# Performance work log

Measured on AMD Instinct MI355X. Metric: run time of the kernel, lower is better.

Reference implementation:

```python
import jax, jax.numpy as jnp
import numpy as np

DIM_CODES = 512
DICT_SIZE = 512
EMBED_DIM = 16
BATCH = 512


def setup_inputs() -> dict:
    key = jax.random.key(0)
    k1, k2 = jax.random.split(key)
    mu = jax.random.normal(k1, (BATCH, DIM_CODES * EMBED_DIM), dtype=jnp.float32)
    dictionary = jax.random.normal(k2, (DIM_CODES, DICT_SIZE, EMBED_DIM), dtype=jnp.float32)
    return {"mu": mu, "dictionary": dictionary}


def reference(mu, dictionary):
    # mu: [B, C*E], dictionary: [C, K, E]
    B = mu.shape[0]
    C, K, E = dictionary.shape
    mu3 = mu.reshape(B, C, E)
    # pairwise squared distance ||mu - d||^2 = ||mu||^2 + ||d||^2 - 2 mu.d -> [B, C, K]
    dist = (jnp.sum(mu3 * mu3, axis=-1)[..., None]
            + jnp.sum(dictionary * dictionary, axis=-1)[None]
            - 2.0 * jnp.einsum('bce,cke->bck', mu3, dictionary))
    idx = jnp.argmin(dist, axis=-1)  # [B, C] int
    # gather nearest codebook entries: per-code index into its own codebook
    z_embed = dictionary[jnp.arange(C)[None, :], idx]  # [B, C, E]
    z_embed = z_embed.reshape(B, C * E)
    # TransferGrad: forward = z_embed, backward passes grad straight-through to mu
    z = mu + jax.lax.stop_gradient(z_embed - mu)
    one_hot_idx = jax.nn.one_hot(idx, K, dtype=mu.dtype)  # [B, C, K]
    return z, z_embed, one_hot_idx
```

## Files before the change

kernel.cpp:

```cpp
#include <hip/hip_runtime.h>
#include <float.h>

constexpr int C    = 512;
constexpr int K    = 512;
constexpr int E    = 16;
constexpr int B    = 512;
constexpr int RB   = 256;
constexpr int MUS  = C * E;

typedef float f32x4 __attribute__((ext_vector_type(4)));

__launch_bounds__(256, 4)
__global__ void vq_scan(const float* __restrict__ mu,
                        const float* __restrict__ dict,
                        float* __restrict__ z,
                        float* __restrict__ zq,
                        int*   __restrict__ idx_t)
{
    const int c    = blockIdx.x;
    const int b0   = blockIdx.y * RB;
    const int tid  = threadIdx.x;
    const int lane = tid & 63;
    const int wave = tid >> 6;

    __shared__ __align__(16) float dict_s[K * E];
    __shared__ float nrm_s[K];

    const float* __restrict__ dbase = dict + (size_t)c * K * E;

#pragma unroll
    for (int rep = 0; rep < 2; ++rep) {
        const int k = tid + rep * 256;
        const float4* p = reinterpret_cast<const float4*>(dbase + k * E);
        const float4 d0 = p[0], d1 = p[1], d2 = p[2], d3 = p[3];
        float s = d0.x * d0.x;
        s = fmaf(d0.y, d0.y, s); s = fmaf(d0.z, d0.z, s); s = fmaf(d0.w, d0.w, s);
        s = fmaf(d1.x, d1.x, s); s = fmaf(d1.y, d1.y, s);
        s = fmaf(d1.z, d1.z, s); s = fmaf(d1.w, d1.w, s);
        s = fmaf(d2.x, d2.x, s); s = fmaf(d2.y, d2.y, s);
        s = fmaf(d2.z, d2.z, s); s = fmaf(d2.w, d2.w, s);
        s = fmaf(d3.x, d3.x, s); s = fmaf(d3.y, d3.y, s);
        s = fmaf(d3.z, d3.z, s); s = fmaf(d3.w, d3.w, s);
        float4* q4 = reinterpret_cast<float4*>(&dict_s[k * E]);
        q4[0] = d0; q4[1] = d1; q4[2] = d2; q4[3] = d3;
        nrm_s[k] = s;
    }
    __syncthreads();

    const int myrow = (wave << 6) + lane;
    const int b     = b0 + myrow;
    const float* __restrict__ mrow = mu + (size_t)b * MUS + c * E;
    float4 m0, m1, m2, m3;
    {
        const float4* p = reinterpret_cast<const float4*>(mrow);
        m0 = p[0]; m1 = p[1]; m2 = p[2]; m3 = p[3];
    }
    float nm = m0.x * m0.x;
    nm = fmaf(m0.y, m0.y, nm); nm = fmaf(m0.z, m0.z, nm); nm = fmaf(m0.w, m0.w, nm);
    nm = fmaf(m1.x, m1.x, nm); nm = fmaf(m1.y, m1.y, nm);
    nm = fmaf(m1.z, m1.z, nm); nm = fmaf(m1.w, m1.w, nm);
    nm = fmaf(m2.x, m2.x, nm); nm = fmaf(m2.y, m2.y, nm);
    nm = fmaf(m2.z, m2.z, nm); nm = fmaf(m2.w, m2.w, nm);
    nm = fmaf(m3.x, m3.x, nm); nm = fmaf(m3.y, m3.y, nm);
    nm = fmaf(m3.z, m3.z, nm); nm = fmaf(m3.w, m3.w, nm);

    float bd = FLT_MAX, sec = FLT_MAX;
    int   bk = K;
    const float4* __restrict__ ds4 = reinterpret_cast<const float4*>(dict_s);
#pragma unroll 4
    for (int k = 0; k < K; ++k) {
        const float4 d0 = ds4[k * 4 + 0];
        const float4 d1 = ds4[k * 4 + 1];
        const float4 d2 = ds4[k * 4 + 2];
        const float4 d3 = ds4[k * 4 + 3];
        float acc = d0.x * m0.x;
        acc = fmaf(d0.y, m0.y, acc); acc = fmaf(d0.z, m0.z, acc); acc = fmaf(d0.w, m0.w, acc);
        acc = fmaf(d1.x, m1.x, acc); acc = fmaf(d1.y, m1.y, acc);
        acc = fmaf(d1.z, m1.z, acc); acc = fmaf(d1.w, m1.w, acc);
        acc = fmaf(d2.x, m2.x, acc); acc = fmaf(d2.y, m2.y, acc);
        acc = fmaf(d2.z, m2.z, acc); acc = fmaf(d2.w, m2.w, acc);
        acc = fmaf(d3.x, m3.x, acc); acc = fmaf(d3.y, m3.y, acc);
        acc = fmaf(d3.z, m3.z, acc); acc = fmaf(d3.w, m3.w, acc);
        const float dist = fmaf(-2.0f, acc, nm + nrm_s[k]);
        const bool  lt   = dist < bd;
        sec = lt ? bd : fminf(sec, dist);
        bd  = lt ? dist : bd;
        bk  = lt ? k : bk;
    }

    unsigned long long trig = __ballot(sec < bd + 1e-3f);
    while (trig) {
        const int r = __ffsll(trig) - 1;
        trig &= trig - 1;
        const int row = (wave << 6) + r;
        const float* __restrict__ qrow = mu + (size_t)(b0 + row) * MUS + c * E;

        double nmuD = 0.0;
#pragma unroll
        for (int t = 0; t < E; ++t) {
            const double mt = (double)qrow[t];
            nmuD += mt * mt;
        }
        double bD = DBL_MAX;
        int    bK = K;
#pragma unroll
        for (int i = 0; i < 8; ++i) {
            const int k = lane + 64 * i;
            const float* dk = &dict_s[k * E];
            double nd = 0.0, dt = 0.0;
#pragma unroll
            for (int t = 0; t < 4; ++t) {
                const double dx = dk[4 * t + 0], dy = dk[4 * t + 1];
                const double dz = dk[4 * t + 2], dw = dk[4 * t + 3];
                const double mx = qrow[4 * t + 0], my = qrow[4 * t + 1];
                const double mz = qrow[4 * t + 2], mw = qrow[4 * t + 3];
                nd += dx * dx + dy * dy + dz * dz + dw * dw;
                dt += dx * mx + dy * my + dz * mz + dw * mw;
            }
            const double dist = nmuD + nd - 2.0 * dt;
            if (dist < bD) { bD = dist; bK = k; }
        }
#pragma unroll
        for (int off = 32; off; off >>= 1) {
            const double od = __shfl_down(bD, off);
            const int    ok = __shfl_down(bK, off);
            if (od < bD || (od == bD && ok < bK)) { bD = od; bK = ok; }
        }
        const int kwin = __shfl(bK, 0);
        if (lane == r) bk = kwin;
    }

    idx_t[c * B + b] = bk;

    {
        const float4* dwin = reinterpret_cast<const float4*>(&dict_s[bk * E]);
        const float4 q0 = dwin[0], q1 = dwin[1], q2 = dwin[2], q3 = dwin[3];
        float* zqp = zq + (size_t)b * MUS + (size_t)c * E;
        float* zp  = z  + (size_t)b * MUS + (size_t)c * E;
        reinterpret_cast<float4*>(zqp)[0] = q0;
        reinterpret_cast<float4*>(zqp)[1] = q1;
        reinterpret_cast<float4*>(zqp)[2] = q2;
        reinterpret_cast<float4*>(zqp)[3] = q3;
        float4 z0, z1, z2, z3;
        z0.x = m0.x + (q0.x - m0.x); z0.y = m0.y + (q0.y - m0.y);
        z0.z = m0.z + (q0.z - m0.z); z0.w = m0.w + (q0.w - m0.w);
        z1.x = m1.x + (q1.x - m1.x); z1.y = m1.y + (q1.y - m1.y);
        z1.z = m1.z + (q1.z - m1.z); z1.w = m1.w + (q1.w - m1.w);
        z2.x = m2.x + (q2.x - m2.x); z2.y = m2.y + (q2.y - m2.y);
        z2.z = m2.z + (q2.z - m2.z); z2.w = m2.w + (q2.w - m2.w);
        z3.x = m3.x + (q3.x - m3.x); z3.y = m3.y + (q3.y - m3.y);
        z3.z = m3.z + (q3.z - m3.z); z3.w = m3.w + (q3.w - m3.w);
        reinterpret_cast<float4*>(zp)[0] = z0;
        reinterpret_cast<float4*>(zp)[1] = z1;
        reinterpret_cast<float4*>(zp)[2] = z2;
        reinterpret_cast<float4*>(zp)[3] = z3;
    }
}

__launch_bounds__(256)
__global__ void vq_onehot(const int* __restrict__ idx_t,
                          float* __restrict__ oh)
{
    const long TOT = (long)B * C * K / 4;
    const long stride = (long)gridDim.x * blockDim.x;
    long f4 = (long)blockIdx.x * blockDim.x + threadIdx.x;
#pragma unroll 4
    for (; f4 < TOT; f4 += stride) {
        const int rowu = __builtin_amdgcn_readfirstlane((int)(f4 >> 7));
        const int bb   = rowu >> 9;
        const int cc   = rowu & (C - 1);
        const int kk   = idx_t[cc * B + bb];
        const int k0   = ((int)f4 & 127) << 2;
        f32x4 v;
        v.x = (k0 + 0 == kk) ? 1.0f : 0.0f;
        v.y = (k0 + 1 == kk) ? 1.0f : 0.0f;
        v.z = (k0 + 2 == kk) ? 1.0f : 0.0f;
        v.w = (k0 + 3 == kk) ? 1.0f : 0.0f;
        __builtin_nontemporal_store(v, reinterpret_cast<f32x4*>(oh) + f4);
    }
}

extern "C" void kernel_launch(void* const* d_in, const int* in_sizes, int n_in,
                              void* d_out, int out_size, void* d_ws, size_t ws_size,
                              hipStream_t stream)
{
    const float* mu   = (const float*)d_in[0];
    const float* dict = (const float*)d_in[1];

    float* z  = (float*)d_out;
    float* zq = z  + (size_t)B * C * E;
    float* oh = zq + (size_t)B * C * E;

    int* idx_t = (int*)d_ws;

    dim3 g1(C, B / RB);
    vq_scan<<<g1, 256, 0, stream>>>(mu, dict, z, zq, idx_t);
    vq_onehot<<<2048, 256, 0, stream>>>(idx_t, oh);
}
```

Before: 701.6 us.

## Register-block four batch rows per thread to reuse each LDS dictionary read

Each thread now handles four batch rows for one code, so every dictionary entry read from LDS feeds four dot products instead of one. The grid drops to one 128-thread block per code, and each block loads its codebook once rather than twice. This cuts LDS traffic per FMA and duplicated dictionary loads. In exchange it raises register pressure, reduces the total thread count to 64K, and lowers occupancy (launch bounds 128,1), which may hurt latency hiding.

```diff
diff --git a/kernel.cpp b/kernel.cpp
--- a/kernel.cpp
+++ b/kernel.cpp
@@ -5,12 +5,12 @@
 constexpr int K    = 512;
 constexpr int E    = 16;
 constexpr int B    = 512;
-constexpr int RB   = 256;
 constexpr int MUS  = C * E;
+constexpr int R    = 4;
 
 typedef float f32x4 __attribute__((ext_vector_type(4)));
 
-__launch_bounds__(256, 4)
+__launch_bounds__(128, 1)
 __global__ void vq_scan(const float* __restrict__ mu,
                         const float* __restrict__ dict,
                         float* __restrict__ z,
@@ -18,7 +18,6 @@
                         int*   __restrict__ idx_t)
 {
     const int c    = blockIdx.x;
-    const int b0   = blockIdx.y * RB;
     const int tid  = threadIdx.x;
     const int lane = tid & 63;
     const int wave = tid >> 6;
@@ -29,8 +28,8 @@
     const float* __restrict__ dbase = dict + (size_t)c * K * E;
 
 #pragma unroll
-    for (int rep = 0; rep < 2; ++rep) {
-        const int k = tid + rep * 256;
+    for (int rep = 0; rep < 4; ++rep) {
+        const int k = tid + rep * 128;
         const float4* p = reinterpret_cast<const float4*>(dbase + k * E);
         const float4 d0 = p[0], d1 = p[1], d2 = p[2], d3 = p[3];
         float s = d0.x * d0.x;
@@ -47,25 +46,33 @@
     }
     __syncthreads();
 
-    const int myrow = (wave << 6) + lane;
-    const int b     = b0 + myrow;
-    const float* __restrict__ mrow = mu + (size_t)b * MUS + c * E;
-    float4 m0, m1, m2, m3;
-    {
-        const float4* p = reinterpret_cast<const float4*>(mrow);
-        m0 = p[0]; m1 = p[1]; m2 = p[2]; m3 = p[3];
-    }
-    float nm = m0.x * m0.x;
-    nm = fmaf(m0.y, m0.y, nm); nm = fmaf(m0.z, m0.z, nm); nm = fmaf(m0.w, m0.w, nm);
-    nm = fmaf(m1.x, m1.x, nm); nm = fmaf(m1.y, m1.y, nm);
-    nm = fmaf(m1.z, m1.z, nm); nm = fmaf(m1.w, m1.w, nm);
-    nm = fmaf(m2.x, m2.x, nm); nm = fmaf(m2.y, m2.y, nm);
-    nm = fmaf(m2.z, m2.z, nm); nm = fmaf(m2.w, m2.w, nm);
-    nm = fmaf(m3.x, m3.x, nm); nm = fmaf(m3.y, m3.y, nm);
-    nm = fmaf(m3.z, m3.z, nm); nm = fmaf(m3.w, m3.w, nm);
-
-    float bd = FLT_MAX, sec = FLT_MAX;
-    int   bk = K;
+    float4 m[R][4];
+    float  nm[R];
+#pragma unroll
+    for (int s = 0; s < R; ++s) {
+        const int b = tid + 128 * s;
+        const float4* p = reinterpret_cast<const float4*>(
+            mu + (size_t)b * MUS + c * E);
+        m[s][0] = p[0]; m[s][1] = p[1]; m[s][2] = p[2]; m[s][3] = p[3];
+        float v = m[s][0].x * m[s][0].x;
+        v = fmaf(m[s][0].y, m[s][0].y, v);
+        v = fmaf(m[s][0].z, m[s][0].z, v);
+        v = fmaf(m[s][0].w, m[s][0].w, v);
+#pragma unroll
+        for (int t = 1; t < 4; ++t) {
+            v = fmaf(m[s][t].x, m[s][t].x, v);
+            v = fmaf(m[s][t].y, m[s][t].y, v);
+            v = fmaf(m[s][t].z, m[s][t].z, v);
+            v = fmaf(m[s][t].w, m[s][t].w, v);
+        }
+        nm[s] = v;
+    }
+
+    float bd[R], sec[R];
+    int   bk[R];
+#pragma unroll
+    for (int s = 0; s < R; ++s) { bd[s] = FLT_MAX; sec[s] = FLT_MAX; bk[s] = K; }
+
     const float4* __restrict__ ds4 = reinterpret_cast<const float4*>(dict_s);
 #pragma unroll 4
     for (int k = 0; k < K; ++k) {
@@ -73,67 +80,84 @@
         const float4 d1 = ds4[k * 4 + 1];
         const float4 d2 = ds4[k * 4 + 2];
         const float4 d3 = ds4[k * 4 + 3];
-        float acc = d0.x * m0.x;
-        acc = fmaf(d0.y, m0.y, acc); acc = fmaf(d0.z, m0.z, acc); acc = fmaf(d0.w, m0.w, acc);
-        acc = fmaf(d1.x, m1.x, acc); acc = fmaf(d1.y, m1.y, acc);
-        acc = fmaf(d1.z, m1.z, acc); acc = fmaf(d1.w, m1.w, acc);
-        acc = fmaf(d2.x, m2.x, acc); acc = fmaf(d2.y, m2.y, acc);
-        acc = fmaf(d2.z, m2.z, acc); acc = fmaf(d2.w, m2.w, acc);
-        acc = fmaf(d3.x, m3.x, acc); acc = fmaf(d3.y, m3.y, acc);
-        acc = fmaf(d3.z, m3.z, acc); acc = fmaf(d3.w, m3.w, acc);
-        const float dist = fmaf(-2.0f, acc, nm + nrm_s[k]);
-        const bool  lt   = dist < bd;
-        sec = lt ? bd : fminf(sec, dist);
-        bd  = lt ? dist : bd;
-        bk  = lt ? k : bk;
-    }
-
-    unsigned long long trig = __ballot(sec < bd + 1e-3f);
-    while (trig) {
-        const int r = __ffsll(trig) - 1;
-        trig &= trig - 1;
-        const int row = (wave << 6) + r;
-        const float* __restrict__ qrow = mu + (size_t)(b0 + row) * MUS + c * E;
-
-        double nmuD = 0.0;
-#pragma unroll
-        for (int t = 0; t < E; ++t) {
-            const double mt = (double)qrow[t];
-            nmuD += mt * mt;
+        const float  nr = nrm_s[k];
+#pragma unroll
+        for (int s = 0; s < R; ++s) {
+            float acc = d0.x * m[s][0].x;
+            acc = fmaf(d0.y, m[s][0].y, acc);
+            acc = fmaf(d0.z, m[s][0].z, acc);
+            acc = fmaf(d0.w, m[s][0].w, acc);
+            acc = fmaf(d1.x, m[s][1].x, acc);
+            acc = fmaf(d1.y, m[s][1].y, acc);
+            acc = fmaf(d1.z, m[s][1].z, acc);
+            acc = fmaf(d1.w, m[s][1].w, acc);
+            acc = fmaf(d2.x, m[s][2].x, acc);
+            acc = fmaf(d2.y, m[s][2].y, acc);
+            acc = fmaf(d2.z, m[s][2].z, acc);
+            acc = fmaf(d2.w, m[s][2].w, acc);
+            acc = fmaf(d3.x, m[s][3].x, acc);
+            acc = fmaf(d3.y, m[s][3].y, acc);
+            acc = fmaf(d3.z, m[s][3].z, acc);
+            acc = fmaf(d3.w, m[s][3].w, acc);
+            const float dist = fmaf(-2.0f, acc, nm[s] + nr);
+            const bool  lt   = dist < bd[s];
+            sec[s] = lt ? bd[s] : fminf(sec[s], dist);
+            bd[s]  = lt ? dist : bd[s];
+            bk[s]  = lt ? k : bk[s];
         }
-        double bD = DBL_MAX;
-        int    bK = K;
-#pragma unroll
-        for (int i = 0; i < 8; ++i) {
-            const int k = lane + 64 * i;
-            const float* dk = &dict_s[k * E];
-            double nd = 0.0, dt = 0.0;
-#pragma unroll
-            for (int t = 0; t < 4; ++t) {
-                const double dx = dk[4 * t + 0], dy = dk[4 * t + 1];
-                const double dz = dk[4 * t + 2], dw = dk[4 * t + 3];
-                const double mx = qrow[4 * t + 0], my = qrow[4 * t + 1];
-                const double mz = qrow[4 * t + 2], mw = qrow[4 * t + 3];
-                nd += dx * dx + dy * dy + dz * dz + dw * dw;
-                dt += dx * mx + dy * my + dz * mz + dw * mw;
+    }
+
+#pragma unroll
+    for (int s = 0; s < R; ++s) {
+        unsigned long long trig = __ballot(sec[s] < bd[s] + 1e-3f);
+        while (trig) {
+            const int r = __ffsll(trig) - 1;
+            trig &= trig - 1;
+            const int row = (wave << 6) + r + 128 * s;
+            const float* __restrict__ qrow = mu + (size_t)row * MUS + c * E;
+
+            double nmuD = 0.0;
+#pragma unroll
+            for (int t = 0; t < E; ++t) {
+                const double mt = (double)qrow[t];
+                nmuD += mt * mt;
             }
-            const double dist = nmuD + nd - 2.0 * dt;
-            if (dist < bD) { bD = dist; bK = k; }
+            double bD = DBL_MAX;
+            int    bK = K;
+#pragma unroll
+            for (int i = 0; i < 8; ++i) {
+                const int kk = lane + 64 * i;
+                const float* dk = &dict_s[kk * E];
+                double nd = 0.0, dt = 0.0;
+#pragma unroll
+                for (int t = 0; t < 4; ++t) {
+                    const double dx = dk[4 * t + 0], dy = dk[4 * t + 1];
+                    const double dz = dk[4 * t + 2], dw = dk[4 * t + 3];
+                    const double mx = qrow[4 * t + 0], my = qrow[4 * t + 1];
+                    const double mz = qrow[4 * t + 2], mw = qrow[4 * t + 3];
+                    nd += dx * dx + dy * dy + dz * dz + dw * dw;
+                    dt += dx * mx + dy * my + dz * mz + dw * mw;
+                }
+                const double dist = nmuD + nd - 2.0 * dt;
+                if (dist < bD) { bD = dist; bK = kk; }
+            }
+#pragma unroll
+            for (int off = 32; off; off >>= 1) {
+                const double od = __shfl_down(bD, off);
+                const int    ok = __shfl_down(bK, off);
+                if (od < bD || (od == bD && ok < bK)) { bD = od; bK = ok; }
+            }
+            const int kwin = __shfl(bK, 0);
+            if (lane == r) bk[s] = kwin;
         }
-#pragma unroll
-        for (int off = 32; off; off >>= 1) {
-            const double od = __shfl_down(bD, off);
-            const int    ok = __shfl_down(bK, off);
-            if (od < bD || (od == bD && ok < bK)) { bD = od; bK = ok; }
-        }
-        const int kwin = __shfl(bK, 0);
-        if (lane == r) bk = kwin;
-    }
-
-    idx_t[c * B + b] = bk;
-
-    {
-        const float4* dwin = reinterpret_cast<const float4*>(&dict_s[bk * E]);
+    }
+
+#pragma unroll
+    for (int s = 0; s < R; ++s) {
+        const int b = tid + 128 * s;
+        idx_t[c * B + b] = bk[s];
+
+        const float4* dwin = reinterpret_cast<const float4*>(&dict_s[bk[s] * E]);
         const float4 q0 = dwin[0], q1 = dwin[1], q2 = dwin[2], q3 = dwin[3];
         float* zqp = zq + (size_t)b * MUS + (size_t)c * E;
         float* zp  = z  + (size_t)b * MUS + (size_t)c * E;
@@ -142,14 +166,14 @@
         reinterpret_cast<float4*>(zqp)[2] = q2;
         reinterpret_cast<float4*>(zqp)[3] = q3;
         float4 z0, z1, z2, z3;
-        z0.x = m0.x + (q0.x - m0.x); z0.y = m0.y + (q0.y - m0.y);
-        z0.z = m0.z + (q0.z - m0.z); z0.w = m0.w + (q0.w - m0.w);
-        z1.x = m1.x + (q1.x - m1.x); z1.y = m1.y + (q1.y - m1.y);
-        z1.z = m1.z + (q1.z - m1.z); z1.w = m1.w + (q1.w - m1.w);
-        z2.x = m2.x + (q2.x - m2.x); z2.y = m2.y + (q2.y - m2.y);
-        z2.z = m2.z + (q2.z - m2.z); z2.w = m2.w + (q2.w - m2.w);
-        z3.x = m3.x + (q3.x - m3.x); z3.y = m3.y + (q3.y - m3.y);
-        z3.z = m3.z + (q3.z - m3.z); z3.w = m3.w + (q3.w - m3.w);
+        z0.x = m[s][0].x + (q0.x - m[s][0].x); z0.y = m[s][0].y + (q0.y - m[s][0].y);
+        z0.z = m[s][0].z + (q0.z - m[s][0].z); z0.w = m[s][0].w + (q0.w - m[s][0].w);
+        z1.x = m[s][1].x + (q1.x - m[s][1].x); z1.y = m[s][1].y + (q1.y - m[s][1].y);
+        z1.z = m[s][1].z + (q1.z - m[s][1].z); z1.w = m[s][1].w + (q1.w - m[s][1].w);
+        z2.x = m[s][2].x + (q2.x - m[s][2].x); z2.y = m[s][2].y + (q2.y - m[s][2].y);
+        z2.z = m[s][2].z + (q2.z - m[s][2].z); z2.w = m[s][2].w + (q2.w - m[s][2].w);
+        z3.x = m[s][3].x + (q3.x - m[s][3].x); z3.y = m[s][3].y + (q3.y - m[s][3].y);
+        z3.z = m[s][3].z + (q3.z - m[s][3].z); z3.w = m[s][3].w + (q3.w - m[s][3].w);
         reinterpret_cast<float4*>(zp)[0] = z0;
         reinterpret_cast<float4*>(zp)[1] = z1;
         reinterpret_cast<float4*>(zp)[2] = z2;
@@ -193,7 +217,6 @@
 
     int* idx_t = (int*)d_ws;
 
-    dim3 g1(C, B / RB);
-    vq_scan<<<g1, 256, 0, stream>>>(mu, dict, z, zq, idx_t);
+    vq_scan<<<dim3(C), 128, 0, stream>>>(mu, dict, z, zq, idx_t);
     vq_onehot<<<2048, 256, 0, stream>>>(idx_t, oh);
 }
```

Result: faster. 669.8 us (-4.5%).

## Compute codebook distances with split-bf16 MFMA instead of scalar FP32 FMAs

Applied to the files above, without the earlier changes.

The scalar per-row dot-product scan is replaced by 32x32x16 bf16 MFMA tiles. Both the dictionary and mu are split into hi and lo bf16 parts, giving near-fp32 accuracy from four MFMAs per tile, and the ||mu||^2 term is dropped from the argmin score. Each block now handles all 512 batch rows for one code, with each wave covering four 32-row tiles. The margin that triggers an fp64 re-check rises to TAU, and that check and the final gather now read the dictionary from global memory. This trades more near-tie fp64 fallbacks and lower occupancy for a much cheaper main distance computation.

```diff
diff --git a/kernel.cpp b/kernel.cpp
--- a/kernel.cpp
+++ b/kernel.cpp
@@ -5,12 +5,24 @@
 constexpr int K    = 512;
 constexpr int E    = 16;
 constexpr int B    = 512;
-constexpr int RB   = 256;
 constexpr int MUS  = C * E;
 
-typedef float f32x4 __attribute__((ext_vector_type(4)));
-
-__launch_bounds__(256, 4)
+#define TAU 2.5e-3f
+
+typedef float f32x4  __attribute__((ext_vector_type(4)));
+typedef __attribute__((ext_vector_type(8)))  short short8;
+typedef __attribute__((ext_vector_type(16))) float f32x16;
+
+__device__ __forceinline__ unsigned short bf16_rne(float f) {
+    unsigned u = __float_as_uint(f);
+    u += 0x7FFFu + ((u >> 16) & 1u);
+    return (unsigned short)(u >> 16);
+}
+__device__ __forceinline__ float bf16_f32(unsigned short h) {
+    return __uint_as_float(((unsigned)h) << 16);
+}
+
+__launch_bounds__(256, 2)
 __global__ void vq_scan(const float* __restrict__ mu,
                         const float* __restrict__ dict,
                         float* __restrict__ z,
@@ -18,12 +30,14 @@
                         int*   __restrict__ idx_t)
 {
     const int c    = blockIdx.x;
-    const int b0   = blockIdx.y * RB;
     const int tid  = threadIdx.x;
     const int lane = tid & 63;
     const int wave = tid >> 6;
-
-    __shared__ __align__(16) float dict_s[K * E];
+    const int lr   = lane & 31;
+    const int lh   = lane >> 5;
+
+    __shared__ __align__(16) unsigned short Ahi[16][64][8];
+    __shared__ __align__(16) unsigned short Alo[16][64][8];
     __shared__ float nrm_s[K];
 
     const float* __restrict__ dbase = dict + (size_t)c * K * E;
@@ -41,119 +55,165 @@
         s = fmaf(d2.z, d2.z, s); s = fmaf(d2.w, d2.w, s);
         s = fmaf(d3.x, d3.x, s); s = fmaf(d3.y, d3.y, s);
         s = fmaf(d3.z, d3.z, s); s = fmaf(d3.w, d3.w, s);
-        float4* q4 = reinterpret_cast<float4*>(&dict_s[k * E]);
-        q4[0] = d0; q4[1] = d1; q4[2] = d2; q4[3] = d3;
         nrm_s[k] = s;
+
+        const float de[16] = { d0.x, d0.y, d0.z, d0.w, d1.x, d1.y, d1.z, d1.w,
+                               d2.x, d2.y, d2.z, d2.w, d3.x, d3.y, d3.z, d3.w };
+        const int kt = k >> 5, kr = k & 31;
+#pragma unroll
+        for (int j = 0; j < 8; ++j) {
+            float f0 = -2.0f * de[j];
+            unsigned short h0 = bf16_rne(f0);
+            Ahi[kt][kr][j] = h0;
+            Alo[kt][kr][j] = bf16_rne(f0 - bf16_f32(h0));
+            float f1 = -2.0f * de[8 + j];
+            unsigned short h1 = bf16_rne(f1);
+            Ahi[kt][32 + kr][j] = h1;
+            Alo[kt][32 + kr][j] = bf16_rne(f1 - bf16_f32(h1));
+        }
     }
     __syncthreads();
 
-    const int myrow = (wave << 6) + lane;
-    const int b     = b0 + myrow;
-    const float* __restrict__ mrow = mu + (size_t)b * MUS + c * E;
-    float4 m0, m1, m2, m3;
-    {
-        const float4* p = reinterpret_cast<const float4*>(mrow);
-        m0 = p[0]; m1 = p[1]; m2 = p[2]; m3 = p[3];
-    }
-    float nm = m0.x * m0.x;
-    nm = fmaf(m0.y, m0.y, nm); nm = fmaf(m0.z, m0.z, nm); nm = fmaf(m0.w, m0.w, nm);
-    nm = fmaf(m1.x, m1.x, nm); nm = fmaf(m1.y, m1.y, nm);
-    nm = fmaf(m1.z, m1.z, nm); nm = fmaf(m1.w, m1.w, nm);
-    nm = fmaf(m2.x, m2.x, nm); nm = fmaf(m2.y, m2.y, nm);
-    nm = fmaf(m2.z, m2.z, nm); nm = fmaf(m2.w, m2.w, nm);
-    nm = fmaf(m3.x, m3.x, nm); nm = fmaf(m3.y, m3.y, nm);
-    nm = fmaf(m3.z, m3.z, nm); nm = fmaf(m3.w, m3.w, nm);
-
-    float bd = FLT_MAX, sec = FLT_MAX;
-    int   bk = K;
-    const float4* __restrict__ ds4 = reinterpret_cast<const float4*>(dict_s);
-#pragma unroll 4
-    for (int k = 0; k < K; ++k) {
-        const float4 d0 = ds4[k * 4 + 0];
-        const float4 d1 = ds4[k * 4 + 1];
-        const float4 d2 = ds4[k * 4 + 2];
-        const float4 d3 = ds4[k * 4 + 3];
-        float acc = d0.x * m0.x;
-        acc = fmaf(d0.y, m0.y, acc); acc = fmaf(d0.z, m0.z, acc); acc = fmaf(d0.w, m0.w, acc);
-        acc = fmaf(d1.x, m1.x, acc); acc = fmaf(d1.y, m1.y, acc);
-        acc = fmaf(d1.z, m1.z, acc); acc = fmaf(d1.w, m1.w, acc);
-        acc = fmaf(d2.x, m2.x, acc); acc = fmaf(d2.y, m2.y, acc);
-        acc = fmaf(d2.z, m2.z, acc); acc = fmaf(d2.w, m2.w, acc);
-        acc = fmaf(d3.x, m3.x, acc); acc = fmaf(d3.y, m3.y, acc);
-        acc = fmaf(d3.z, m3.z, acc); acc = fmaf(d3.w, m3.w, acc);
-        const float dist = fmaf(-2.0f, acc, nm + nrm_s[k]);
-        const bool  lt   = dist < bd;
-        sec = lt ? bd : fminf(sec, dist);
-        bd  = lt ? dist : bd;
-        bk  = lt ? k : bk;
-    }
-
-    unsigned long long trig = __ballot(sec < bd + 1e-3f);
-    while (trig) {
-        const int r = __ffsll(trig) - 1;
-        trig &= trig - 1;
-        const int row = (wave << 6) + r;
-        const float* __restrict__ qrow = mu + (size_t)(b0 + row) * MUS + c * E;
-
-        double nmuD = 0.0;
-#pragma unroll
-        for (int t = 0; t < E; ++t) {
-            const double mt = (double)qrow[t];
-            nmuD += mt * mt;
-        }
-        double bD = DBL_MAX;
-        int    bK = K;
-#pragma unroll
-        for (int i = 0; i < 8; ++i) {
-            const int k = lane + 64 * i;
-            const float* dk = &dict_s[k * E];
-            double nd = 0.0, dt = 0.0;
-#pragma unroll
-            for (int t = 0; t < 4; ++t) {
-                const double dx = dk[4 * t + 0], dy = dk[4 * t + 1];
-                const double dz = dk[4 * t + 2], dw = dk[4 * t + 3];
-                const double mx = qrow[4 * t + 0], my = qrow[4 * t + 1];
-                const double mz = qrow[4 * t + 2], mw = qrow[4 * t + 3];
-                nd += dx * dx + dy * dy + dz * dz + dw * dw;
-                dt += dx * mx + dy * my + dz * mz + dw * mw;
-            }
-            const double dist = nmuD + nd - 2.0 * dt;
-            if (dist < bD) { bD = dist; bK = k; }
-        }
-#pragma unroll
-        for (int off = 32; off; off >>= 1) {
-            const double od = __shfl_down(bD, off);
-            const int    ok = __shfl_down(bK, off);
-            if (od < bD || (od == bD && ok < bK)) { bD = od; bK = ok; }
-        }
-        const int kwin = __shfl(bK, 0);
-        if (lane == r) bk = kwin;
-    }
-
-    idx_t[c * B + b] = bk;
-
-    {
-        const float4* dwin = reinterpret_cast<const float4*>(&dict_s[bk * E]);
-        const float4 q0 = dwin[0], q1 = dwin[1], q2 = dwin[2], q3 = dwin[3];
-        float* zqp = zq + (size_t)b * MUS + (size_t)c * E;
-        float* zp  = z  + (size_t)b * MUS + (size_t)c * E;
-        reinterpret_cast<float4*>(zqp)[0] = q0;
-        reinterpret_cast<float4*>(zqp)[1] = q1;
-        reinterpret_cast<float4*>(zqp)[2] = q2;
-        reinterpret_cast<float4*>(zqp)[3] = q3;
-        float4 z0, z1, z2, z3;
-        z0.x = m0.x + (q0.x - m0.x); z0.y = m0.y + (q0.y - m0.y);
-        z0.z = m0.z + (q0.z - m0.z); z0.w = m0.w + (q0.w - m0.w);
-        z1.x = m1.x + (q1.x - m1.x); z1.y = m1.y + (q1.y - m1.y);
-        z1.z = m1.z + (q1.z - m1.z); z1.w = m1.w + (q1.w - m1.w);
-        z2.x = m2.x + (q2.x - m2.x); z2.y = m2.y + (q2.y - m2.y);
-        z2.z = m2.z + (q2.z - m2.z); z2.w = m2.w + (q2.w - m2.w);
-        z3.x = m3.x + (q3.x - m3.x); z3.y = m3.y + (q3.y - m3.y);
-        z3.z = m3.z + (q3.z - m3.z); z3.w = m3.w + (q3.w - m3.w);
-        reinterpret_cast<float4*>(zp)[0] = z0;
-        reinterpret_cast<float4*>(zp)[1] = z1;
-        reinterpret_cast<float4*>(zp)[2] = z2;
-        reinterpret_cast<float4*>(zp)[3] = z3;
+    short8 bh[4], bl[4];
+#pragma unroll
+    for (int j = 0; j < 4; ++j) {
+        const int bt = wave * 4 + j;
+        const int b  = bt * 32 + lr;
+        const float4* mp = reinterpret_cast<const float4*>(
+            mu + (size_t)b * MUS + c * E + lh * 8);
+        const float4 x0 = mp[0], x1 = mp[1];
+        const float me[8] = { x0.x, x0.y, x0.z, x0.w, x1.x, x1.y, x1.z, x1.w };
+        unsigned short hh[8], ll[8];
+#pragma unroll
+        for (int e = 0; e < 8; ++e) {
+            hh[e] = bf16_rne(me[e]);
+            ll[e] = bf16_rne(me[e] - bf16_f32(hh[e]));
+        }
+        bh[j] = *reinterpret_cast<const short8*>(hh);
+        bl[j] = *reinterpret_cast<const short8*>(ll);
+    }
+
+    float bd[4], sec[4];
+    int   bk[4];
+#pragma unroll
+    for (int j = 0; j < 4; ++j) { bd[j] = FLT_MAX; sec[j] = FLT_MAX; bk[j] = K; }
+
+    for (int kt = 0; kt < 16; ++kt) {
+        const short8 ah = *reinterpret_cast<const short8*>(&Ahi[kt][lane][0]);
+        const short8 al = *reinterpret_cast<const short8*>(&Alo[kt][lane][0]);
+        float nr[16];
+#pragma unroll
+        for (int r = 0; r < 16; ++r)
+            nr[r] = nrm_s[kt * 32 + (r & 3) + 8 * (r >> 2) + 4 * lh];
+
+#pragma unroll
+        for (int j = 0; j < 4; ++j) {
+            f32x16 acc = {};
+            acc = __builtin_amdgcn_mfma_f32_32x32x16_bf16(ah, bh[j], acc, 0, 0, 0);
+            acc = __builtin_amdgcn_mfma_f32_32x32x16_bf16(ah, bl[j], acc, 0, 0, 0);
+            acc = __builtin_amdgcn_mfma_f32_32x32x16_bf16(al, bh[j], acc, 0, 0, 0);
+            acc = __builtin_amdgcn_mfma_f32_32x32x16_bf16(al, bl[j], acc, 0, 0, 0);
+#pragma unroll
+            for (int r = 0; r < 16; ++r) {
+                const float S = acc[r] + nr[r];
+                const int   k = kt * 32 + (r & 3) + 8 * (r >> 2) + 4 * lh;
+                const bool  lt = S < bd[j];
+                sec[j] = lt ? bd[j] : fminf(sec[j], S);
+                bd[j]  = lt ? S : bd[j];
+                bk[j]  = lt ? k : bk[j];
+            }
+        }
+    }
+
+#pragma unroll
+    for (int j = 0; j < 4; ++j) {
+        const float od = __shfl_xor(bd[j], 32);
+        const float os = __shfl_xor(sec[j], 32);
+        const int   ok = __shfl_xor(bk[j], 32);
+        if (od < bd[j] || (od == bd[j] && ok < bk[j])) {
+            sec[j] = fminf(bd[j], os); bd[j] = od; bk[j] = ok;
+        } else {
+            sec[j] = fminf(sec[j], od);
+        }
+    }
+
+#pragma unroll
+    for (int j = 0; j < 4; ++j) {
+        const int bt = wave * 4 + j;
+
+        unsigned long long trig = __ballot(lane < 32 && (sec[j] - bd[j] < TAU));
+        while (trig) {
+            const int r = __ffsll(trig) - 1;
+            trig &= trig - 1;
+            const int row = bt * 32 + r;
+            const float* __restrict__ qrow = mu + (size_t)row * MUS + c * E;
+
+            double nmuD = 0.0;
+#pragma unroll
+            for (int t = 0; t < E; ++t) {
+                const double mt = (double)qrow[t];
+                nmuD += mt * mt;
+            }
+            double bD = DBL_MAX;
+            int    bK = K;
+#pragma unroll
+            for (int i = 0; i < 8; ++i) {
+                const int kk = lane + 64 * i;
+                const float* dk = dbase + (size_t)kk * E;
+                double nd = 0.0, dt = 0.0;
+#pragma unroll
+                for (int t = 0; t < 4; ++t) {
+                    const double dx = dk[4 * t + 0], dy = dk[4 * t + 1];
+                    const double dz = dk[4 * t + 2], dw = dk[4 * t + 3];
+                    const double mx = qrow[4 * t + 0], my = qrow[4 * t + 1];
+                    const double mz = qrow[4 * t + 2], mw = qrow[4 * t + 3];
+                    nd += dx * dx + dy * dy + dz * dz + dw * dw;
+                    dt += dx * mx + dy * my + dz * mz + dw * mw;
+                }
+                const double dist = nmuD + nd - 2.0 * dt;
+                if (dist < bD) { bD = dist; bK = kk; }
+            }
+#pragma unroll
+            for (int off = 32; off; off >>= 1) {
+                const double od = __shfl_down(bD, off);
+                const int    ok = __shfl_down(bK, off);
+                if (od < bD || (od == bD && ok < bK)) { bD = od; bK = ok; }
+            }
+            const int kwin = __shfl(bK, 0);
+            if (lane == r) bk[j] = kwin;
+        }
+
+        if (lane < 32) {
+            const int b = bt * 32 + lane;
+            idx_t[c * B + b] = bk[j];
+
+            const float4* mp = reinterpret_cast<const float4*>(
+                mu + (size_t)b * MUS + c * E);
+            const float4 m0 = mp[0], m1 = mp[1], m2 = mp[2], m3 = mp[3];
+            const float4* dwin = reinterpret_cast<const float4*>(
+                dbase + (size_t)bk[j] * E);
+            const float4 q0 = dwin[0], q1 = dwin[1], q2 = dwin[2], q3 = dwin[3];
+
+            float* zqp = zq + (size_t)b * MUS + (size_t)c * E;
+            float* zp  = z  + (size_t)b * MUS + (size_t)c * E;
+            reinterpret_cast<float4*>(zqp)[0] = q0;
+            reinterpret_cast<float4*>(zqp)[1] = q1;
+            reinterpret_cast<float4*>(zqp)[2] = q2;
+            reinterpret_cast<float4*>(zqp)[3] = q3;
+            float4 z0, z1, z2, z3;
+            z0.x = m0.x + (q0.x - m0.x); z0.y = m0.y + (q0.y - m0.y);
+            z0.z = m0.z + (q0.z - m0.z); z0.w = m0.w + (q0.w - m0.w);
+            z1.x = m1.x + (q1.x - m1.x); z1.y = m1.y + (q1.y - m1.y);
+            z1.z = m1.z + (q1.z - m1.z); z1.w = m1.w + (q1.w - m1.w);
+            z2.x = m2.x + (q2.x - m2.x); z2.y = m2.y + (q2.y - m2.y);
+            z2.z = m2.z + (q2.z - m2.z); z2.w = m2.w + (q2.w - m2.w);
+            z3.x = m3.x + (q3.x - m3.x); z3.y = m3.y + (q3.y - m3.y);
+            z3.z = m3.z + (q3.z - m3.z); z3.w = m3.w + (q3.w - m3.w);
+            reinterpret_cast<float4*>(zp)[0] = z0;
+            reinterpret_cast<float4*>(zp)[1] = z1;
+            reinterpret_cast<float4*>(zp)[2] = z2;
+            reinterpret_cast<float4*>(zp)[3] = z3;
+        }
     }
 }
 
@@ -193,7 +253,6 @@
 
     int* idx_t = (int*)d_ws;
 
-    dim3 g1(C, B / RB);
-    vq_scan<<<g1, 256, 0, stream>>>(mu, dict, z, zq, idx_t);
+    vq_scan<<<dim3(C), 256, 0, stream>>>(mu, dict, z, zq, idx_t);
     vq_onehot<<<2048, 256, 0, stream>>>(idx_t, oh);
 }
```

New measurement: 647.3 us. 1.08x faster.
